# Kernel tuning notes

Measured on AMD Instinct MI355X. Metric: run time of the kernel, lower is better.

The kernel has to match this reference:

```python
import jax, jax.numpy as jnp
import numpy as np

# --- constants derived from init_kwargs (mirrors Categorical2DSemanticMapModule.__init__) ---
H, W = 480, 640
HFOV = 79
DU = 4                      # du_scale
NSEM = 16                   # num_sem_categories
VR = 100                    # vision_range
XY_RES = Z_RES = 5          # map_resolution (cm per bin)
MIN_DEPTH, MAX_DEPTH = 20.0, 500.0   # cm (0.2m/5.0m * 100)
AGENT_H = 88.0              # camera_height * 100 cm
MIN_VOX = int(-40 / Z_RES)  # -8
MAX_VOX = int(360 / Z_RES)  # 72
ZBINS = MAX_VOX - MIN_VOX   # 80
MIN_MAPPED = int(25 / Z_RES - MIN_VOX)             # 13 (min_obs_height_cm)
MAX_MAPPED = int((AGENT_H + 1) / Z_RES - MIN_VOX)  # 25
MAP_T, EXP_T, CAT_T = 1.0, 1.0, 5.0                # map/exp/cat pred thresholds
DILATE_ITER, DILATE_SIZE = 1, 3
F_PIX = (W / 2.0) / float(np.tan(np.deg2rad(HFOV / 2.0)))
CX, CY = W / 2.0, H / 2.0
B, T = 4, 4
LM = 240   # local map size
GM = 960   # global map size
NMAP = 4 + NSEM  # NON_SEM_CHANNELS + num_sem_categories


def setup_inputs() -> dict:
    key = jax.random.key(0)
    k1, k2 = jax.random.split(key)
    seq_obs = jax.random.uniform(k1, (B, T, 4 + NSEM, H, W), dtype=jnp.float32)
    seq_obs = seq_obs.at[:, :, 3].multiply(600.0)  # depth channel in cm, spans [0, 600)
    seq_pose_delta = jax.random.normal(k2, (B, T, 3), dtype=jnp.float32) * 0.1
    seq_camera_poses = jnp.tile(jnp.eye(4, dtype=jnp.float32)[None], (B, 1, 1))
    return {
        'seq_obs': seq_obs,
        'seq_pose_delta': seq_pose_delta,
        'seq_dones': jnp.zeros((B, T), jnp.int32),
        'seq_update_global': jnp.ones((B, T), jnp.int32),
        'seq_camera_poses': seq_camera_poses,
        'init_local_map': jnp.zeros((B, NMAP, LM, LM), jnp.float32),
        'init_global_map': jnp.zeros((B, NMAP, GM, GM), jnp.float32),
        'init_local_pose': jnp.zeros((B, 3), jnp.float32),
        'init_global_pose': jnp.zeros((B, 3), jnp.float32),
        'init_lmb': jnp.zeros((B, 4), jnp.int32),
        'init_origins': jnp.zeros((B, 3), jnp.float32),
    }


def _ego_map(obs_bt):
    """Core semantic-mapping kernel for one frame.
    obs_bt: (4+NSEM, H, W) -> ego map (2+NSEM, VR, VR).
    depth -> point cloud -> voxel scatter-add -> height projection -> threshold -> dilation.
    """
    depth = obs_bt[3, ::DU, ::DU]        # (h, w) cm
    sem = obs_bt[4:, ::DU, ::DU]         # (NSEM, h, w)
    h, w = depth.shape
    uu, vv = jnp.meshgrid(jnp.arange(w, dtype=jnp.float32) * DU,
                          jnp.arange(h, dtype=jnp.float32) * DU)
    # pinhole back-projection (cm), camera at agent height, elevation 0
    X = (uu - CX) * depth / F_PIX            # lateral
    Zh = AGENT_H + (CY - vv) * depth / F_PIX  # height above floor
    Yf = depth                                # forward range
    valid = (depth > MIN_DEPTH) & (depth < MAX_DEPTH)
    # voxel binning (shift_loc centers agent laterally at VR/2)
    xb = jnp.round(X / XY_RES + VR / 2.0).astype(jnp.int32)
    yb = jnp.round(Yf / XY_RES).astype(jnp.int32)
    zb = jnp.round(Zh / Z_RES).astype(jnp.int32) - MIN_VOX
    valid = valid & (xb >= 0) & (xb < VR) & (yb >= 0) & (yb < VR) & (zb >= 0) & (zb < ZBINS)
    lin = (yb * VR + xb) * ZBINS + zb
    lin = jnp.where(valid, lin, VR * VR * ZBINS)  # route invalid points to a dump bin
    C = 1 + NSEM
    feat = jnp.concatenate([jnp.ones((1, h, w), depth.dtype), sem], 0)  # (C, h, w)
    feat = jnp.where(valid[None], feat, 0.0).reshape(C, -1).T           # (N, C)
    grid = jnp.zeros((VR * VR * ZBINS + 1, C), feat.dtype).at[lin.reshape(-1)].add(feat)
    vox = grid[:-1].reshape(VR, VR, ZBINS, C)
    agent_h = vox[:, :, MIN_MAPPED:MAX_MAPPED].sum(2)  # (VR, VR, C)
    all_h = vox.sum(2)
    obstacle = jnp.clip(agent_h[..., 0] / MAP_T, 0.0, 1.0)
    explored = jnp.clip(all_h[..., 0] / EXP_T, 0.0, 1.0)
    semmap = jnp.clip(all_h[..., 1:] / CAT_T, 0.0, 1.0)
    # morphological dilation of obstacle map (3x3 max, dilate_iter times)
    for _ in range(DILATE_ITER):
        obstacle = jax.lax.reduce_window(obstacle, 0.0, jax.lax.max,
                                         (DILATE_SIZE, DILATE_SIZE), (1, 1), 'SAME')
    return jnp.concatenate([obstacle[None], explored[None], jnp.moveaxis(semmap, -1, 0)], 0)


def reference(seq_obs, seq_pose_delta, seq_dones, seq_update_global, seq_camera_poses,
              init_local_map, init_global_map, init_local_pose, init_global_pose,
              init_lmb, init_origins):
    Bb, Tt = seq_obs.shape[:2]
    flat = seq_obs.reshape((Bb * Tt,) + seq_obs.shape[2:])
    ego = jax.vmap(_ego_map)(flat)                      # (B*T, 2+NSEM, VR, VR)
    return ego.reshape(Bb, Tt, 2 + NSEM, VR, VR)
```

## Files before the change

### kernel.cpp

```cpp
#include <hip/hip_runtime.h>
#include <math.h>

#define IMG_H 480
#define IMG_W 640
#define DU    4
#define SUB_H 120
#define SUB_W 160
#define NPIX  (SUB_H * SUB_W)
#define NSEM  16
#define NCH_IN 20
#define VR    100
#define ZBINS 80
#define MIN_MAPPED 13
#define MAX_MAPPED 25
#define NOUT  18
#define NCELL (VR * VR)
#define NJOBS 16
#define BLOCK 1024

__global__ __launch_bounds__(BLOCK, 1)
void ego_map_kernel(const float* __restrict__ obs,
                    float* __restrict__ out,
                    float f_pix, int nframes) {
    __shared__ float acc[NCELL];
    __shared__ float acc2[NCELL];

    const int f = blockIdx.x % nframes;
    const int j = blockIdx.x / nframes;
    const int tid = threadIdx.x;

    for (int c = tid; c < NCELL; c += BLOCK) acc[c] = 0.0f;
    if (j < 2)
        for (int c = tid; c < NCELL; c += BLOCK) acc2[c] = 0.0f;
    __syncthreads();

    const float* frame    = obs + (size_t)f * NCH_IN * IMG_H * IMG_W;
    const float* depth_ch = frame + (size_t)3 * IMG_H * IMG_W;
    const float* sem_ch   = frame + (size_t)(4 + j) * IMG_H * IMG_W;

    for (int p = tid; p < NPIX; p += BLOCK) {
        int v = p / SUB_W;
        int u = p - v * SUB_W;
        size_t pix = (size_t)(v * DU) * IMG_W + (size_t)(u * DU);

        float depth = depth_ch[pix];
        if (!(depth > 20.0f && depth < 500.0f)) continue;

        float uu = (float)(u * DU);
        float vv = (float)(v * DU);
        float X  = (uu - 320.0f) * depth / f_pix;
        float Zh = 88.0f + (240.0f - vv) * depth / f_pix;

        int xb = (int)rintf(X / 5.0f + 50.0f);
        int yb = (int)rintf(depth / 5.0f);
        int zb = (int)rintf(Zh / 5.0f) + 8;

        if (xb < 0 || xb >= VR || yb < 0 || yb >= VR || zb < 0 || zb >= ZBINS)
            continue;

        int cell = yb * VR + xb;
        float s = __builtin_nontemporal_load(sem_ch + pix);
        atomicAdd(&acc[cell], s);
        if (j == 0) {
            if (zb >= MIN_MAPPED && zb < MAX_MAPPED)
                acc2[cell] = 1.0f;
        } else if (j == 1) {
            acc2[cell] = 1.0f;
        }
    }
    __syncthreads();

    float* outf = out + (size_t)f * NOUT * NCELL;

    {
        float* oc = outf + (size_t)(2 + j) * NCELL;
        for (int c = tid; c < NCELL; c += BLOCK) {
            float val = fminf(fmaxf(acc[c] / 5.0f, 0.0f), 1.0f);
            __builtin_nontemporal_store(val, oc + c);
        }
    }

    if (j == 0) {
        for (int c = tid; c < NCELL; c += BLOCK) {
            int y = c / VR;
            int x = c - y * VR;
            float m = 0.0f;
            int y0 = (y > 0) ? y - 1 : 0, y1 = (y < VR - 1) ? y + 1 : VR - 1;
            int x0 = (x > 0) ? x - 1 : 0, x1 = (x < VR - 1) ? x + 1 : VR - 1;
            for (int yy = y0; yy <= y1; ++yy)
                for (int xx = x0; xx <= x1; ++xx)
                    m = fmaxf(m, acc2[yy * VR + xx]);
            __builtin_nontemporal_store(fminf(m, 1.0f), outf + c);
        }
    } else if (j == 1) {
        for (int c = tid; c < NCELL; c += BLOCK) {
            float val = fminf(fmaxf(acc2[c], 0.0f), 1.0f);
            __builtin_nontemporal_store(val, outf + NCELL + c);
        }
    }
}

extern "C" void kernel_launch(void* const* d_in, const int* in_sizes, int n_in,
                              void* d_out, int out_size, void* d_ws, size_t ws_size,
                              hipStream_t stream) {
    const float* obs = (const float*)d_in[0];
    float* out = (float*)d_out;

    int nframes = in_sizes[0] / (NCH_IN * IMG_H * IMG_W);

    float f_pix = (float)(IMG_W / 2.0 / tan((79.0 / 2.0) * M_PI / 180.0));

    ego_map_kernel<<<nframes * NJOBS, BLOCK, 0, stream>>>(obs, out, f_pix, nframes);
}
```

Measured before the change: 593.4 us.

## Split depth binning into a separate pass and share packed cell records

Per-pixel depth projection and voxel binning moves into its own kernel. That kernel writes one packed int per subsampled pixel, holding the cell index plus valid and agent-height flags, into workspace. The scatter kernel then reads these records instead of each of the 16 per-channel blocks re-reading depth and recomputing the projection. It also skips the semantic load for invalid pixels with no depth math. The cost is an extra kernel launch and a workspace round trip.

```diff
diff --git a/kernel.cpp b/kernel.cpp
--- a/kernel.cpp
+++ b/kernel.cpp
@@ -17,11 +17,58 @@
 #define NCELL (VR * VR)
 #define NJOBS 16
 #define BLOCK 1024
+#define NSLICE 16
+
+#define REC_VALID (1 << 16)
+#define REC_AGENT (1 << 17)
+
 
 __global__ __launch_bounds__(BLOCK, 1)
-void ego_map_kernel(const float* __restrict__ obs,
+void binning_kernel(const float* __restrict__ obs,
+                    int* __restrict__ recs,
+                    float f_pix, int nframes) {
+    const int f = blockIdx.x % nframes;
+    const int s = blockIdx.x / nframes;
+    const int tid = threadIdx.x;
+
+    const float* depth_ch = obs + ((size_t)f * NCH_IN + 3) * IMG_H * IMG_W;
+    int* rec = recs + (size_t)f * NPIX;
+
+    const int p0 = s * (NPIX / NSLICE);
+    const int p1 = p0 + NPIX / NSLICE;
+
+    for (int p = p0 + tid; p < p1; p += BLOCK) {
+        int v = p / SUB_W;
+        int u = p - v * SUB_W;
+        size_t pix = (size_t)(v * DU) * IMG_W + (size_t)(u * DU);
+
+        float depth = depth_ch[pix];
+        int r = 0;
+        if (depth > 20.0f && depth < 500.0f) {
+            float uu = (float)(u * DU);
+            float vv = (float)(v * DU);
+            float X  = (uu - 320.0f) * depth / f_pix;
+            float Zh = 88.0f + (240.0f - vv) * depth / f_pix;
+
+            int xb = (int)rintf(X / 5.0f + 50.0f);
+            int yb = (int)rintf(depth / 5.0f);
+            int zb = (int)rintf(Zh / 5.0f) + 8;
+
+            if (xb >= 0 && xb < VR && yb >= 0 && yb < VR &&
+                zb >= 0 && zb < ZBINS) {
+                r = (yb * VR + xb) | REC_VALID;
+                if (zb >= MIN_MAPPED && zb < MAX_MAPPED) r |= REC_AGENT;
+            }
+        }
+        rec[p] = r;
+    }
+}
+
+__global__ __launch_bounds__(BLOCK, 1)
+void scatter_kernel(const float* __restrict__ obs,
+                    const int* __restrict__ recs,
                     float* __restrict__ out,
-                    float f_pix, int nframes) {
+                    int nframes) {
     __shared__ float acc[NCELL];
     __shared__ float acc2[NCELL];
 
@@ -34,35 +81,22 @@
         for (int c = tid; c < NCELL; c += BLOCK) acc2[c] = 0.0f;
     __syncthreads();
 
-    const float* frame    = obs + (size_t)f * NCH_IN * IMG_H * IMG_W;
-    const float* depth_ch = frame + (size_t)3 * IMG_H * IMG_W;
-    const float* sem_ch   = frame + (size_t)(4 + j) * IMG_H * IMG_W;
+    const float* sem_ch = obs + ((size_t)f * NCH_IN + 4 + j) * IMG_H * IMG_W;
+    const int* rec = recs + (size_t)f * NPIX;
 
     for (int p = tid; p < NPIX; p += BLOCK) {
+        int r = rec[p];
+        if (!(r & REC_VALID)) continue;
+
         int v = p / SUB_W;
         int u = p - v * SUB_W;
         size_t pix = (size_t)(v * DU) * IMG_W + (size_t)(u * DU);
 
-        float depth = depth_ch[pix];
-        if (!(depth > 20.0f && depth < 500.0f)) continue;
-
-        float uu = (float)(u * DU);
-        float vv = (float)(v * DU);
-        float X  = (uu - 320.0f) * depth / f_pix;
-        float Zh = 88.0f + (240.0f - vv) * depth / f_pix;
-
-        int xb = (int)rintf(X / 5.0f + 50.0f);
-        int yb = (int)rintf(depth / 5.0f);
-        int zb = (int)rintf(Zh / 5.0f) + 8;
-
-        if (xb < 0 || xb >= VR || yb < 0 || yb >= VR || zb < 0 || zb >= ZBINS)
-            continue;
-
-        int cell = yb * VR + xb;
+        int cell = r & 0xFFFF;
         float s = __builtin_nontemporal_load(sem_ch + pix);
         atomicAdd(&acc[cell], s);
         if (j == 0) {
-            if (zb >= MIN_MAPPED && zb < MAX_MAPPED)
+            if (r & REC_AGENT)
                 acc2[cell] = 1.0f;
         } else if (j == 1) {
             acc2[cell] = 1.0f;
@@ -105,10 +139,12 @@
                               hipStream_t stream) {
     const float* obs = (const float*)d_in[0];
     float* out = (float*)d_out;
+    int* recs = (int*)d_ws;
 
     int nframes = in_sizes[0] / (NCH_IN * IMG_H * IMG_W);
 
     float f_pix = (float)(IMG_W / 2.0 / tan((79.0 / 2.0) * M_PI / 180.0));
 
-    ego_map_kernel<<<nframes * NJOBS, BLOCK, 0, stream>>>(obs, out, f_pix, nframes);
+    binning_kernel<<<nframes * NSLICE, BLOCK, 0, stream>>>(obs, recs, f_pix, nframes);
+    scatter_kernel<<<nframes * NJOBS, BLOCK, 0, stream>>>(obs, recs, out, nframes);
 }
```

Result: no change. 595.4 us (+0.3%).
